# Optimization experiments

Hardware: AMD Instinct MI355X
Metric: run time of the kernel (lower is better)

The kernel has to match this reference:

```python
import jax, jax.numpy as jnp
import numpy as np

B, TE, TD, D, U = 8, 256, 256, 256, 256


def setup_inputs() -> dict:
    key = jax.random.key(0)
    k1, k2, k3, k4, k5 = jax.random.split(key, 5)
    glorot = lambda k, shape: jax.random.uniform(
        k, shape, jnp.float32,
        -np.sqrt(6.0 / (shape[0] + shape[1])), np.sqrt(6.0 / (shape[0] + shape[1])))
    return {
        "en_seq": jax.random.normal(k1, (B, TE, D), jnp.float32),
        "de_seq": jax.random.normal(k2, (B, TD, D), jnp.float32),
        "w_en": glorot(k3, (D, U)),
        "w_de": glorot(k4, (D, U)),
        "nu": glorot(k5, (U, 1)),
    }


def reference(en_seq, de_seq, w_en, w_de, nu):
    # Additive co-attention scores.
    ae = jnp.einsum('bte,eu->btu', en_seq, w_en)          # (B, Te, U)
    ad = jnp.einsum('bsd,du->bsu', de_seq, w_de)          # (B, Td, U)
    # co_m[b, td, te, u] = ae[b, te, u] + ad[b, td, u]  (matches K.repeat / repeat_elements layout)
    co = jnp.tanh(ad[:, :, None, :] + ae[:, None, :, :])  # (B, Td, Te, U)
    mu = jnp.einsum('bstu,ul->bst', co, nu)               # (B, Td, Te)
    alphas = jax.nn.softmax(mu, axis=-1)                  # softmax over en time
    max_mu = jnp.max(mu, axis=-1)                         # (B, Td)
    max_alphas = jax.nn.softmax(max_mu, axis=-1)          # softmax over de time
    h_hat = jnp.sum(de_seq * max_alphas[..., None], axis=1)  # (B, Dd)
    sum_en = jnp.einsum('bst,bte->bse', alphas, en_seq)      # (B, Td, De)
    output = jnp.concatenate(
        [de_seq, sum_en, de_seq * sum_en, de_seq * h_hat[:, None, :]], axis=-1)
    return output  # (B, Td, 4*D)
```

## Files before the change

kernel.cpp:

```cpp
#include <hip/hip_runtime.h>

#define B_   8
#define TE_  256
#define TD_  256
#define D_   256
#define U_   256

#define AE_OFF    0
#define AD_OFF    524288
#define MU_OFF    1048576
#define MAXMU_OFF 1572864
#define HH_OFF    1574912

__device__ __forceinline__ float fexp2(float x) {
#if __has_builtin(__builtin_amdgcn_exp2f)
  return __builtin_amdgcn_exp2f(x);
#else
  return exp2f(x);
#endif
}
__device__ __forceinline__ float frcp(float x) {
#if __has_builtin(__builtin_amdgcn_rcpf)
  return __builtin_amdgcn_rcpf(x);
#else
  return 1.0f / x;
#endif
}

#define LOG2E_F 1.4426950408889634f
#define TWO_LOG2E_F 2.8853900817779268f

__global__ __launch_bounds__(256) void coatt_k1_proj(
    const float* __restrict__ en, const float* __restrict__ de,
    const float* __restrict__ w_en, const float* __restrict__ w_de,
    float* __restrict__ ws) {
  const int which = blockIdx.z;
  const float* __restrict__ A = which ? de : en;
  const float* __restrict__ W = which ? w_de : w_en;
  float* __restrict__ out = ws + (which ? AD_OFF : AE_OFF);
  const int rowBase = blockIdx.y * 64;
  const int colBase = blockIdx.x * 64;
  __shared__ float As[16][68];
  __shared__ float Bs[16][68];
  const int tid = threadIdx.x;
  const int tx = tid & 15, ty = tid >> 4;
  float acc[4][4] = {};
  for (int k0 = 0; k0 < D_; k0 += 16) {
    {
      const int r = tid >> 2;
      const int c = (tid & 3) * 4;
      const float4 a4 = *(const float4*)&A[(rowBase + r) * D_ + k0 + c];
      As[c + 0][r] = a4.x; As[c + 1][r] = a4.y;
      As[c + 2][r] = a4.z; As[c + 3][r] = a4.w;
      const int kk = tid >> 4;
      const int cc = (tid & 15) * 4;
      *(float4*)&Bs[kk][cc] = *(const float4*)&W[(k0 + kk) * U_ + colBase + cc];
    }
    __syncthreads();
#pragma unroll
    for (int k = 0; k < 16; ++k) {
      float av[4], bv[4];
      *(float4*)av = *(const float4*)&As[k][ty * 4];
      *(float4*)bv = *(const float4*)&Bs[k][tx * 4];
#pragma unroll
      for (int i = 0; i < 4; ++i)
#pragma unroll
        for (int j = 0; j < 4; ++j)
          acc[i][j] = fmaf(av[i], bv[j], acc[i][j]);
    }
    __syncthreads();
  }
#pragma unroll
  for (int i = 0; i < 4; ++i) {
    float4 o;
    o.x = fexp2(acc[i][0] * TWO_LOG2E_F);
    o.y = fexp2(acc[i][1] * TWO_LOG2E_F);
    o.z = fexp2(acc[i][2] * TWO_LOG2E_F);
    o.w = fexp2(acc[i][3] * TWO_LOG2E_F);
    *(float4*)&out[(rowBase + ty * 4 + i) * U_ + colBase + tx * 4] = o;
  }
}

__global__ __launch_bounds__(256) void coatt_k2_mu(
    const float* __restrict__ nu, float* __restrict__ ws) {
  const float* __restrict__ ae = ws + AE_OFF;
  const float* __restrict__ ad = ws + AD_OFF;
  float* __restrict__ mu = ws + MU_OFF;
  const int b = blockIdx.z;
  const int sBase = blockIdx.y * 32;
  const int tBase = blockIdx.x * 32;
  __shared__ float ADs[32][20];
  __shared__ float AEs[32][20];
  __shared__ float NUs[16];
  const int tid = threadIdx.x;
  const int tx = tid & 15;
  const int sy = tid >> 4;
  float acc00 = 0.f, acc01 = 0.f, acc10 = 0.f, acc11 = 0.f;
  for (int u0 = 0; u0 < U_; u0 += 16) {
    {
      const int r = (tid & 127) >> 2;
      const int c = (tid & 3) * 4;
      if (tid < 128)
        *(float4*)&ADs[r][c] = *(const float4*)&ad[(b * TD_ + sBase + r) * U_ + u0 + c];
      else
        *(float4*)&AEs[r][c] = *(const float4*)&ae[(b * TE_ + tBase + r) * U_ + u0 + c];
      if (tid < 4) {
        const float4 n4 = *(const float4*)&nu[u0 + tid * 4];
        NUs[tid * 4 + 0] = -2.0f * n4.x;
        NUs[tid * 4 + 1] = -2.0f * n4.y;
        NUs[tid * 4 + 2] = -2.0f * n4.z;
        NUs[tid * 4 + 3] = -2.0f * n4.w;
      }
    }
    __syncthreads();
    const float4* A0 = (const float4*)&ADs[sy][0];
    const float4* A1 = (const float4*)&ADs[sy + 16][0];
    const float4* E0 = (const float4*)&AEs[tx][0];
    const float4* E1 = (const float4*)&AEs[tx + 16][0];
    const float4* N4 = (const float4*)&NUs[0];
#pragma unroll
    for (int q = 0; q < 4; ++q) {
      float a0v[4], a1v[4], e0v[4], e1v[4], nv[4];
      *(float4*)a0v = A0[q];
      *(float4*)a1v = A1[q];
      *(float4*)e0v = E0[q];
      *(float4*)e1v = E1[q];
      *(float4*)nv  = N4[q];
#pragma unroll
      for (int u = 0; u < 4; ++u) {
        const float r00 = frcp(fmaf(a0v[u], e0v[u], 1.0f));
        const float r01 = frcp(fmaf(a0v[u], e1v[u], 1.0f));
        const float r10 = frcp(fmaf(a1v[u], e0v[u], 1.0f));
        const float r11 = frcp(fmaf(a1v[u], e1v[u], 1.0f));
        acc00 = fmaf(nv[u], r00, acc00);
        acc01 = fmaf(nv[u], r01, acc01);
        acc10 = fmaf(nv[u], r10, acc10);
        acc11 = fmaf(nv[u], r11, acc11);
      }
    }
    __syncthreads();
  }
  const int s0 = sBase + sy, s1 = s0 + 16;
  const int t0 = tBase + tx, t1 = t0 + 16;
  mu[(b * TD_ + s0) * TE_ + t0] = acc00;
  mu[(b * TD_ + s0) * TE_ + t1] = acc01;
  mu[(b * TD_ + s1) * TE_ + t0] = acc10;
  mu[(b * TD_ + s1) * TE_ + t1] = acc11;
}

__global__ __launch_bounds__(256) void coatt_k3_softmax(float* __restrict__ ws) {
  float* __restrict__ mu = ws + MU_OFF;
  float* __restrict__ maxmu = ws + MAXMU_OFF;
  const int tid = threadIdx.x;
  const int wave = tid >> 6, lane = tid & 63;
  const int row = blockIdx.x * 4 + wave;
  float4 v = *(const float4*)&mu[row * TE_ + lane * 4];
  float m = fmaxf(fmaxf(v.x, v.y), fmaxf(v.z, v.w));
#pragma unroll
  for (int off = 32; off > 0; off >>= 1) m = fmaxf(m, __shfl_xor(m, off));
  float4 e;
  e.x = fexp2((v.x - m) * LOG2E_F);
  e.y = fexp2((v.y - m) * LOG2E_F);
  e.z = fexp2((v.z - m) * LOG2E_F);
  e.w = fexp2((v.w - m) * LOG2E_F);
  float s = (e.x + e.y) + (e.z + e.w);
#pragma unroll
  for (int off = 32; off > 0; off >>= 1) s += __shfl_xor(s, off);
  const float inv = frcp(s);
  e.x *= inv; e.y *= inv; e.z *= inv; e.w *= inv;
  *(float4*)&mu[row * TE_ + lane * 4] = e;
  if (lane == 0) maxmu[row] = m;
}

__global__ __launch_bounds__(256) void coatt_k4_hhat(
    const float* __restrict__ de, float* __restrict__ ws) {
  const float* __restrict__ maxmu = ws + MAXMU_OFF;
  float* __restrict__ hhat = ws + HH_OFF;
  const int b = blockIdx.y;
  const int dBase = blockIdx.x * 32;
  const int tid = threadIdx.x;
  __shared__ float red[256];
  __shared__ float malpha[256];
  const float v = maxmu[b * TD_ + tid];
  red[tid] = v;
  __syncthreads();
  for (int w = 128; w > 0; w >>= 1) {
    if (tid < w) red[tid] = fmaxf(red[tid], red[tid + w]);
    __syncthreads();
  }
  const float m = red[0];
  __syncthreads();
  const float e = fexp2((v - m) * LOG2E_F);
  red[tid] = e;
  __syncthreads();
  for (int w = 128; w > 0; w >>= 1) {
    if (tid < w) red[tid] += red[tid + w];
    __syncthreads();
  }
  malpha[tid] = e * frcp(red[0]);
  __syncthreads();
  const int dl = tid & 31, sg = tid >> 5;
  float acc = 0.f;
  for (int s = sg * 32; s < sg * 32 + 32; ++s)
    acc = fmaf(de[(b * TD_ + s) * D_ + dBase + dl], malpha[s], acc);
  red[tid] = acc;
  __syncthreads();
  if (tid < 32) {
    float t = red[tid];
#pragma unroll
    for (int g = 1; g < 8; ++g) t += red[g * 32 + tid];
    hhat[b * D_ + dBase + tid] = t;
  }
}

__global__ __launch_bounds__(256) void coatt_k5_out(
    const float* __restrict__ en, const float* __restrict__ de,
    const float* __restrict__ ws, float* __restrict__ out) {
  const float* __restrict__ alphas = ws + MU_OFF;
  const float* __restrict__ hhat = ws + HH_OFF;
  const int b = blockIdx.z;
  const int sBase = blockIdx.y * 32;
  const int eBase = blockIdx.x * 32;
  __shared__ float As[16][36];
  __shared__ float Bs[16][36];
  const int tid = threadIdx.x;
  const int tx = tid & 15, sy = tid >> 4;
  float acc[2][2] = {};
  for (int k0 = 0; k0 < TE_; k0 += 16) {
    if (tid < 128) {
      const int r = tid >> 2, c = (tid & 3) * 4;
      const float4 a4 = *(const float4*)&alphas[(b * TD_ + sBase + r) * TE_ + k0 + c];
      As[c + 0][r] = a4.x; As[c + 1][r] = a4.y;
      As[c + 2][r] = a4.z; As[c + 3][r] = a4.w;
    } else {
      const int id = tid & 127;
      const int kk = id >> 3, cc = (id & 7) * 4;
      *(float4*)&Bs[kk][cc] = *(const float4*)&en[(b * TE_ + k0 + kk) * D_ + eBase + cc];
    }
    __syncthreads();
#pragma unroll
    for (int k = 0; k < 16; ++k) {
      const float2 a2 = *(const float2*)&As[k][sy * 2];
      const float2 b2 = *(const float2*)&Bs[k][tx * 2];
      acc[0][0] = fmaf(a2.x, b2.x, acc[0][0]);
      acc[0][1] = fmaf(a2.x, b2.y, acc[0][1]);
      acc[1][0] = fmaf(a2.y, b2.x, acc[1][0]);
      acc[1][1] = fmaf(a2.y, b2.y, acc[1][1]);
    }
    __syncthreads();
  }
  const int e0 = eBase + tx * 2;
  const float2 hh = *(const float2*)&hhat[b * D_ + e0];
#pragma unroll
  for (int i = 0; i < 2; ++i) {
    const int s = sBase + sy * 2 + i;
    const float2 d2 = *(const float2*)&de[(b * TD_ + s) * D_ + e0];
    float* o = out + (size_t)(b * TD_ + s) * (4 * D_);
    float2 se; se.x = acc[i][0]; se.y = acc[i][1];
    *(float2*)&o[e0] = d2;
    *(float2*)&o[D_ + e0] = se;
    float2 p; p.x = d2.x * se.x; p.y = d2.y * se.y;
    *(float2*)&o[2 * D_ + e0] = p;
    float2 q; q.x = d2.x * hh.x; q.y = d2.y * hh.y;
    *(float2*)&o[3 * D_ + e0] = q;
  }
}

extern "C" void kernel_launch(void* const* d_in, const int* in_sizes, int n_in,
                              void* d_out, int out_size, void* d_ws, size_t ws_size,
                              hipStream_t stream) {
  (void)in_sizes; (void)n_in; (void)out_size; (void)ws_size;
  const float* en   = (const float*)d_in[0];
  const float* de   = (const float*)d_in[1];
  const float* w_en = (const float*)d_in[2];
  const float* w_de = (const float*)d_in[3];
  const float* nu   = (const float*)d_in[4];
  float* out = (float*)d_out;
  float* ws  = (float*)d_ws;

  coatt_k1_proj<<<dim3(4, 32, 2), 256, 0, stream>>>(en, de, w_en, w_de, ws);
  coatt_k2_mu<<<dim3(8, 8, 8), 256, 0, stream>>>(nu, ws);
  coatt_k3_softmax<<<dim3(512), 256, 0, stream>>>(ws);
  coatt_k4_hhat<<<dim3(8, 8), 256, 0, stream>>>(de, ws);
  coatt_k5_out<<<dim3(8, 8, 8), 256, 0, stream>>>(en, de, ws, out);
}
```

Measured before the change: 122.6 us.

## Fuse mu, softmax and alpha-weighted en sum into one kernel per decoder tile

Merges the mu score computation, the row softmax and the alphas@en product into a single kernel that keeps each block's 4 decoder rows of scores in shared memory, so the B*Td*Te mu matrix never goes through global memory. The h_hat reduction is folded into the output kernel, which recomputes it per block, cutting the chain from five launches to three. In exchange each block streams the full per-batch Ee and en tensors with only 4 decoder rows of reuse, and the output kernel repeats the h_hat reduction over de in every block.

Measured after the change: 132.4 us. +8.0%, slower.

```diff
diff --git a/kernel.cpp b/kernel.cpp
--- a/kernel.cpp
+++ b/kernel.cpp
@@ -8,9 +8,8 @@
 
 #define AE_OFF    0
 #define AD_OFF    524288
-#define MU_OFF    1048576
+#define SUMEN_OFF 1048576
 #define MAXMU_OFF 1572864
-#define HH_OFF    1574912
 
 __device__ __forceinline__ float fexp2(float x) {
 #if __has_builtin(__builtin_amdgcn_exp2f)
@@ -30,7 +29,7 @@
 #define LOG2E_F 1.4426950408889634f
 #define TWO_LOG2E_F 2.8853900817779268f
 
-__global__ __launch_bounds__(256) void coatt_k1_proj(
+__global__ __launch_bounds__(256) void coatt_ka_proj(
     const float* __restrict__ en, const float* __restrict__ de,
     const float* __restrict__ w_en, const float* __restrict__ w_de,
     float* __restrict__ ws) {
@@ -81,188 +80,191 @@
   }
 }
 
-__global__ __launch_bounds__(256) void coatt_k2_mu(
-    const float* __restrict__ nu, float* __restrict__ ws) {
-  const float* __restrict__ ae = ws + AE_OFF;
-  const float* __restrict__ ad = ws + AD_OFF;
-  float* __restrict__ mu = ws + MU_OFF;
-  const int b = blockIdx.z;
-  const int sBase = blockIdx.y * 32;
-  const int tBase = blockIdx.x * 32;
-  __shared__ float ADs[32][20];
-  __shared__ float AEs[32][20];
-  __shared__ float NUs[16];
+__global__ __launch_bounds__(256) void coatt_kb_fused(
+    const float* __restrict__ nu, const float* __restrict__ en,
+    float* __restrict__ ws) {
+  const float* __restrict__ Ee = ws + AE_OFF;
+  const float* __restrict__ Ed = ws + AD_OFF;
+  float* __restrict__ sum_en = ws + SUMEN_OFF;
+  float* __restrict__ maxmu = ws + MAXMU_OFF;
+  const int b = blockIdx.y;
+  const int sBase = blockIdx.x * 4;
   const int tid = threadIdx.x;
-  const int tx = tid & 15;
-  const int sy = tid >> 4;
-  float acc00 = 0.f, acc01 = 0.f, acc10 = 0.f, acc11 = 0.f;
+  const int w = tid >> 6, lane = tid & 63;
+
+  __shared__ float EdS[4][256];
+  __shared__ float NUs[256];
+  __shared__ float EeT[16][260];
+  __shared__ float Mu[4][260];
+
+  {
+    const int r = tid >> 6, c4 = tid & 63;
+    *(float4*)&EdS[r][c4 * 4] =
+        *(const float4*)&Ed[(b * TD_ + sBase + r) * U_ + c4 * 4];
+    NUs[tid] = -2.0f * nu[tid];
+  }
+  __syncthreads();
+
+  float acc0 = 0.f, acc1 = 0.f, acc2 = 0.f, acc3 = 0.f;
+  const int t = tid;
   for (int u0 = 0; u0 < U_; u0 += 16) {
-    {
-      const int r = (tid & 127) >> 2;
-      const int c = (tid & 3) * 4;
-      if (tid < 128)
-        *(float4*)&ADs[r][c] = *(const float4*)&ad[(b * TD_ + sBase + r) * U_ + u0 + c];
-      else
-        *(float4*)&AEs[r][c] = *(const float4*)&ae[(b * TE_ + tBase + r) * U_ + u0 + c];
-      if (tid < 4) {
-        const float4 n4 = *(const float4*)&nu[u0 + tid * 4];
-        NUs[tid * 4 + 0] = -2.0f * n4.x;
-        NUs[tid * 4 + 1] = -2.0f * n4.y;
-        NUs[tid * 4 + 2] = -2.0f * n4.z;
-        NUs[tid * 4 + 3] = -2.0f * n4.w;
+#pragma unroll
+    for (int k = 0; k < 4; ++k) {
+      const int f = tid + 256 * k;
+      const int tt = f >> 2, c = f & 3;
+      const float4 v = *(const float4*)&Ee[(b * TE_ + tt) * U_ + u0 + c * 4];
+      EeT[c * 4 + 0][tt] = v.x;
+      EeT[c * 4 + 1][tt] = v.y;
+      EeT[c * 4 + 2][tt] = v.z;
+      EeT[c * 4 + 3][tt] = v.w;
+    }
+    __syncthreads();
+#pragma unroll
+    for (int uq = 0; uq < 4; ++uq) {
+      float nv[4];
+      *(float4*)nv = *(const float4*)&NUs[u0 + uq * 4];
+      float ee[4];
+#pragma unroll
+      for (int j = 0; j < 4; ++j) ee[j] = EeT[uq * 4 + j][t];
+      float e0[4], e1[4], e2[4], e3[4];
+      *(float4*)e0 = *(const float4*)&EdS[0][u0 + uq * 4];
+      *(float4*)e1 = *(const float4*)&EdS[1][u0 + uq * 4];
+      *(float4*)e2 = *(const float4*)&EdS[2][u0 + uq * 4];
+      *(float4*)e3 = *(const float4*)&EdS[3][u0 + uq * 4];
+#pragma unroll
+      for (int j = 0; j < 4; ++j) {
+        acc0 = fmaf(nv[j], frcp(fmaf(e0[j], ee[j], 1.0f)), acc0);
+        acc1 = fmaf(nv[j], frcp(fmaf(e1[j], ee[j], 1.0f)), acc1);
+        acc2 = fmaf(nv[j], frcp(fmaf(e2[j], ee[j], 1.0f)), acc2);
+        acc3 = fmaf(nv[j], frcp(fmaf(e3[j], ee[j], 1.0f)), acc3);
       }
     }
     __syncthreads();
-    const float4* A0 = (const float4*)&ADs[sy][0];
-    const float4* A1 = (const float4*)&ADs[sy + 16][0];
-    const float4* E0 = (const float4*)&AEs[tx][0];
-    const float4* E1 = (const float4*)&AEs[tx + 16][0];
-    const float4* N4 = (const float4*)&NUs[0];
-#pragma unroll
-    for (int q = 0; q < 4; ++q) {
-      float a0v[4], a1v[4], e0v[4], e1v[4], nv[4];
-      *(float4*)a0v = A0[q];
-      *(float4*)a1v = A1[q];
-      *(float4*)e0v = E0[q];
-      *(float4*)e1v = E1[q];
-      *(float4*)nv  = N4[q];
-#pragma unroll
-      for (int u = 0; u < 4; ++u) {
-        const float r00 = frcp(fmaf(a0v[u], e0v[u], 1.0f));
-        const float r01 = frcp(fmaf(a0v[u], e1v[u], 1.0f));
-        const float r10 = frcp(fmaf(a1v[u], e0v[u], 1.0f));
-        const float r11 = frcp(fmaf(a1v[u], e1v[u], 1.0f));
-        acc00 = fmaf(nv[u], r00, acc00);
-        acc01 = fmaf(nv[u], r01, acc01);
-        acc10 = fmaf(nv[u], r10, acc10);
-        acc11 = fmaf(nv[u], r11, acc11);
-      }
-    }
-    __syncthreads();
-  }
-  const int s0 = sBase + sy, s1 = s0 + 16;
-  const int t0 = tBase + tx, t1 = t0 + 16;
-  mu[(b * TD_ + s0) * TE_ + t0] = acc00;
-  mu[(b * TD_ + s0) * TE_ + t1] = acc01;
-  mu[(b * TD_ + s1) * TE_ + t0] = acc10;
-  mu[(b * TD_ + s1) * TE_ + t1] = acc11;
-}
-
-__global__ __launch_bounds__(256) void coatt_k3_softmax(float* __restrict__ ws) {
-  float* __restrict__ mu = ws + MU_OFF;
-  float* __restrict__ maxmu = ws + MAXMU_OFF;
+  }
+
+  Mu[0][t] = acc0;
+  Mu[1][t] = acc1;
+  Mu[2][t] = acc2;
+  Mu[3][t] = acc3;
+  __syncthreads();
+  {
+    float4 v = *(const float4*)&Mu[w][lane * 4];
+    float m = fmaxf(fmaxf(v.x, v.y), fmaxf(v.z, v.w));
+#pragma unroll
+    for (int off = 32; off > 0; off >>= 1) m = fmaxf(m, __shfl_xor(m, off));
+    float4 e;
+    e.x = fexp2((v.x - m) * LOG2E_F);
+    e.y = fexp2((v.y - m) * LOG2E_F);
+    e.z = fexp2((v.z - m) * LOG2E_F);
+    e.w = fexp2((v.w - m) * LOG2E_F);
+    float sm = (e.x + e.y) + (e.z + e.w);
+#pragma unroll
+    for (int off = 32; off > 0; off >>= 1) sm += __shfl_xor(sm, off);
+    const float inv = frcp(sm);
+    e.x *= inv; e.y *= inv; e.z *= inv; e.w *= inv;
+    *(float4*)&Mu[w][lane * 4] = e;
+    if (lane == 0) maxmu[b * TD_ + sBase + w] = m;
+  }
+  __syncthreads();
+
+  float4 p0 = {0, 0, 0, 0}, p1 = {0, 0, 0, 0}, p2 = {0, 0, 0, 0}, p3 = {0, 0, 0, 0};
+  for (int t0 = 0; t0 < TE_; t0 += 16) {
+#pragma unroll
+    for (int k = 0; k < 4; ++k) {
+      const int f = tid + 256 * k;
+      const int r = f >> 6, c4 = f & 63;
+      *(float4*)&EeT[r][c4 * 4] =
+          *(const float4*)&en[(b * TE_ + t0 + r) * D_ + c4 * 4];
+    }
+    __syncthreads();
+    float a0[4], a1[4], a2[4], a3[4];
+    *(float4*)a0 = *(const float4*)&Mu[0][t0 + w * 4];
+    *(float4*)a1 = *(const float4*)&Mu[1][t0 + w * 4];
+    *(float4*)a2 = *(const float4*)&Mu[2][t0 + w * 4];
+    *(float4*)a3 = *(const float4*)&Mu[3][t0 + w * 4];
+#pragma unroll
+    for (int j = 0; j < 4; ++j) {
+      const float4 env = *(const float4*)&EeT[w * 4 + j][lane * 4];
+      p0.x = fmaf(a0[j], env.x, p0.x); p0.y = fmaf(a0[j], env.y, p0.y);
+      p0.z = fmaf(a0[j], env.z, p0.z); p0.w = fmaf(a0[j], env.w, p0.w);
+      p1.x = fmaf(a1[j], env.x, p1.x); p1.y = fmaf(a1[j], env.y, p1.y);
+      p1.z = fmaf(a1[j], env.z, p1.z); p1.w = fmaf(a1[j], env.w, p1.w);
+      p2.x = fmaf(a2[j], env.x, p2.x); p2.y = fmaf(a2[j], env.y, p2.y);
+      p2.z = fmaf(a2[j], env.z, p2.z); p2.w = fmaf(a2[j], env.w, p2.w);
+      p3.x = fmaf(a3[j], env.x, p3.x); p3.y = fmaf(a3[j], env.y, p3.y);
+      p3.z = fmaf(a3[j], env.z, p3.z); p3.w = fmaf(a3[j], env.w, p3.w);
+    }
+    __syncthreads();
+  }
+  {
+    float* RED = &EeT[0][0];
+    *(float4*)&RED[((w * 4 + 0) * 64 + lane) * 4] = p0;
+    *(float4*)&RED[((w * 4 + 1) * 64 + lane) * 4] = p1;
+    *(float4*)&RED[((w * 4 + 2) * 64 + lane) * 4] = p2;
+    *(float4*)&RED[((w * 4 + 3) * 64 + lane) * 4] = p3;
+    __syncthreads();
+    const int s = tid >> 6, l = tid & 63;
+    float4 sum = {0, 0, 0, 0};
+#pragma unroll
+    for (int ww = 0; ww < 4; ++ww) {
+      const float4 q = *(const float4*)&RED[((ww * 4 + s) * 64 + l) * 4];
+      sum.x += q.x; sum.y += q.y; sum.z += q.z; sum.w += q.w;
+    }
+    *(float4*)&sum_en[(b * TD_ + sBase + s) * D_ + l * 4] = sum;
+  }
+}
+
+__global__ __launch_bounds__(256) void coatt_kc_out(
+    const float* __restrict__ de, const float* __restrict__ ws,
+    float* __restrict__ out) {
+  const float* __restrict__ sum_en = ws + SUMEN_OFF;
+  const float* __restrict__ maxmu = ws + MAXMU_OFF;
+  const int b = blockIdx.y;
+  const int sBase = blockIdx.x * 8;
   const int tid = threadIdx.x;
-  const int wave = tid >> 6, lane = tid & 63;
-  const int row = blockIdx.x * 4 + wave;
-  float4 v = *(const float4*)&mu[row * TE_ + lane * 4];
-  float m = fmaxf(fmaxf(v.x, v.y), fmaxf(v.z, v.w));
+  const int w = tid >> 6, lane = tid & 63;
+  __shared__ float malpha[256];
+  __shared__ float red[8];
+  __shared__ float hhL[256];
+  const float v = maxmu[b * TD_ + tid];
+  float m = v;
 #pragma unroll
   for (int off = 32; off > 0; off >>= 1) m = fmaxf(m, __shfl_xor(m, off));
-  float4 e;
-  e.x = fexp2((v.x - m) * LOG2E_F);
-  e.y = fexp2((v.y - m) * LOG2E_F);
-  e.z = fexp2((v.z - m) * LOG2E_F);
-  e.w = fexp2((v.w - m) * LOG2E_F);
-  float s = (e.x + e.y) + (e.z + e.w);
-#pragma unroll
-  for (int off = 32; off > 0; off >>= 1) s += __shfl_xor(s, off);
-  const float inv = frcp(s);
-  e.x *= inv; e.y *= inv; e.z *= inv; e.w *= inv;
-  *(float4*)&mu[row * TE_ + lane * 4] = e;
-  if (lane == 0) maxmu[row] = m;
-}
-
-__global__ __launch_bounds__(256) void coatt_k4_hhat(
-    const float* __restrict__ de, float* __restrict__ ws) {
-  const float* __restrict__ maxmu = ws + MAXMU_OFF;
-  float* __restrict__ hhat = ws + HH_OFF;
-  const int b = blockIdx.y;
-  const int dBase = blockIdx.x * 32;
-  const int tid = threadIdx.x;
-  __shared__ float red[256];
-  __shared__ float malpha[256];
-  const float v = maxmu[b * TD_ + tid];
-  red[tid] = v;
-  __syncthreads();
-  for (int w = 128; w > 0; w >>= 1) {
-    if (tid < w) red[tid] = fmaxf(red[tid], red[tid + w]);
-    __syncthreads();
-  }
-  const float m = red[0];
-  __syncthreads();
+  if (lane == 0) red[w] = m;
+  __syncthreads();
+  m = fmaxf(fmaxf(red[0], red[1]), fmaxf(red[2], red[3]));
   const float e = fexp2((v - m) * LOG2E_F);
-  red[tid] = e;
-  __syncthreads();
-  for (int w = 128; w > 0; w >>= 1) {
-    if (tid < w) red[tid] += red[tid + w];
-    __syncthreads();
-  }
-  malpha[tid] = e * frcp(red[0]);
-  __syncthreads();
-  const int dl = tid & 31, sg = tid >> 5;
-  float acc = 0.f;
-  for (int s = sg * 32; s < sg * 32 + 32; ++s)
-    acc = fmaf(de[(b * TD_ + s) * D_ + dBase + dl], malpha[s], acc);
-  red[tid] = acc;
-  __syncthreads();
-  if (tid < 32) {
-    float t = red[tid];
-#pragma unroll
-    for (int g = 1; g < 8; ++g) t += red[g * 32 + tid];
-    hhat[b * D_ + dBase + tid] = t;
-  }
-}
-
-__global__ __launch_bounds__(256) void coatt_k5_out(
-    const float* __restrict__ en, const float* __restrict__ de,
-    const float* __restrict__ ws, float* __restrict__ out) {
-  const float* __restrict__ alphas = ws + MU_OFF;
-  const float* __restrict__ hhat = ws + HH_OFF;
-  const int b = blockIdx.z;
-  const int sBase = blockIdx.y * 32;
-  const int eBase = blockIdx.x * 32;
-  __shared__ float As[16][36];
-  __shared__ float Bs[16][36];
-  const int tid = threadIdx.x;
-  const int tx = tid & 15, sy = tid >> 4;
-  float acc[2][2] = {};
-  for (int k0 = 0; k0 < TE_; k0 += 16) {
-    if (tid < 128) {
-      const int r = tid >> 2, c = (tid & 3) * 4;
-      const float4 a4 = *(const float4*)&alphas[(b * TD_ + sBase + r) * TE_ + k0 + c];
-      As[c + 0][r] = a4.x; As[c + 1][r] = a4.y;
-      As[c + 2][r] = a4.z; As[c + 3][r] = a4.w;
-    } else {
-      const int id = tid & 127;
-      const int kk = id >> 3, cc = (id & 7) * 4;
-      *(float4*)&Bs[kk][cc] = *(const float4*)&en[(b * TE_ + k0 + kk) * D_ + eBase + cc];
-    }
-    __syncthreads();
-#pragma unroll
-    for (int k = 0; k < 16; ++k) {
-      const float2 a2 = *(const float2*)&As[k][sy * 2];
-      const float2 b2 = *(const float2*)&Bs[k][tx * 2];
-      acc[0][0] = fmaf(a2.x, b2.x, acc[0][0]);
-      acc[0][1] = fmaf(a2.x, b2.y, acc[0][1]);
-      acc[1][0] = fmaf(a2.y, b2.x, acc[1][0]);
-      acc[1][1] = fmaf(a2.y, b2.y, acc[1][1]);
-    }
-    __syncthreads();
-  }
-  const int e0 = eBase + tx * 2;
-  const float2 hh = *(const float2*)&hhat[b * D_ + e0];
-#pragma unroll
-  for (int i = 0; i < 2; ++i) {
-    const int s = sBase + sy * 2 + i;
-    const float2 d2 = *(const float2*)&de[(b * TD_ + s) * D_ + e0];
+  float sm = e;
+#pragma unroll
+  for (int off = 32; off > 0; off >>= 1) sm += __shfl_xor(sm, off);
+  if (lane == 0) red[4 + w] = sm;
+  __syncthreads();
+  sm = (red[4] + red[5]) + (red[6] + red[7]);
+  malpha[tid] = e * frcp(sm);
+  __syncthreads();
+  float hh = 0.f;
+#pragma unroll 8
+  for (int s = 0; s < TD_; ++s)
+    hh = fmaf(de[(b * TD_ + s) * D_ + tid], malpha[s], hh);
+  hhL[tid] = hh;
+  __syncthreads();
+#pragma unroll
+  for (int pass = 0; pass < 2; ++pass) {
+    const int s = sBase + pass * 4 + w;
+    const float4 d4 = *(const float4*)&de[(b * TD_ + s) * D_ + lane * 4];
+    const float4 se4 = *(const float4*)&sum_en[(b * TD_ + s) * D_ + lane * 4];
+    const float4 hh4 = *(const float4*)&hhL[lane * 4];
     float* o = out + (size_t)(b * TD_ + s) * (4 * D_);
-    float2 se; se.x = acc[i][0]; se.y = acc[i][1];
-    *(float2*)&o[e0] = d2;
-    *(float2*)&o[D_ + e0] = se;
-    float2 p; p.x = d2.x * se.x; p.y = d2.y * se.y;
-    *(float2*)&o[2 * D_ + e0] = p;
-    float2 q; q.x = d2.x * hh.x; q.y = d2.y * hh.y;
-    *(float2*)&o[3 * D_ + e0] = q;
+    *(float4*)&o[lane * 4] = d4;
+    *(float4*)&o[D_ + lane * 4] = se4;
+    float4 pr;
+    pr.x = d4.x * se4.x; pr.y = d4.y * se4.y;
+    pr.z = d4.z * se4.z; pr.w = d4.w * se4.w;
+    *(float4*)&o[2 * D_ + lane * 4] = pr;
+    float4 q;
+    q.x = d4.x * hh4.x; q.y = d4.y * hh4.y;
+    q.z = d4.z * hh4.z; q.w = d4.w * hh4.w;
+    *(float4*)&o[3 * D_ + lane * 4] = q;
   }
 }
 
@@ -278,9 +280,7 @@
   float* out = (float*)d_out;
   float* ws  = (float*)d_ws;
 
-  coatt_k1_proj<<<dim3(4, 32, 2), 256, 0, stream>>>(en, de, w_en, w_de, ws);
-  coatt_k2_mu<<<dim3(8, 8, 8), 256, 0, stream>>>(nu, ws);
-  coatt_k3_softmax<<<dim3(512), 256, 0, stream>>>(ws);
-  coatt_k4_hhat<<<dim3(8, 8), 256, 0, stream>>>(de, ws);
-  coatt_k5_out<<<dim3(8, 8, 8), 256, 0, stream>>>(en, de, ws, out);
-}
+  coatt_ka_proj<<<dim3(4, 32, 2), 256, 0, stream>>>(en, de, w_en, w_de, ws);
+  coatt_kb_fused<<<dim3(64, 8), 256, 0, stream>>>(nu, en, ws);
+  coatt_kc_out<<<dim3(32, 8), 256, 0, stream>>>(de, ws, out);
+}
```
